# Optimization experiments

Hardware: AMD Instinct MI355X
Metric: run time of the kernel (lower is better)

Reference implementation:

```python
import jax, jax.numpy as jnp
import numpy as np

N = 50000      # nodes
E = 800000     # edges (avg degree 16)
F_IN = 512     # input features
H = 64         # hidden
C = 40         # classes
L = 4          # FAConv layers
EPS = 0.2      # args.epsilon


def setup_inputs() -> dict:
    key = jax.random.key(0)
    ks = jax.random.split(key, 8)
    gain = 1.414
    x = jax.random.normal(ks[0], (N, F_IN), jnp.float32)
    edge_index = jax.random.randint(ks[1], (2, E), 0, N, dtype=jnp.int32)
    W1 = jax.random.normal(ks[2], (H, F_IN), jnp.float32) * (gain * np.sqrt(2.0 / (F_IN + H)))
    b1 = jnp.zeros((H,), jnp.float32)
    W2 = jax.random.normal(ks[3], (C, H), jnp.float32) * (gain * np.sqrt(2.0 / (H + C)))
    b2 = jnp.zeros((C,), jnp.float32)
    att_l = jax.random.normal(ks[4], (L, H), jnp.float32) * np.sqrt(2.0 / (1 + H))
    att_r = jax.random.normal(ks[5], (L, H), jnp.float32) * np.sqrt(2.0 / (1 + H))
    return {"x": x, "edge_index": edge_index, "W1": W1, "b1": b1,
            "W2": W2, "b2": b2, "att_l": att_l, "att_r": att_r}


def reference(x, edge_index, W1, b1, W2, b2, att_l, att_r):
    n = x.shape[0]
    src, dst = edge_index[0], edge_index[1]
    # gcn_norm with self-loops (FAConv normalize=True, add_self_loops=True)
    loop = jnp.arange(n, dtype=src.dtype)
    rows = jnp.concatenate([src, loop])  # source j
    cols = jnp.concatenate([dst, loop])  # target i
    deg = jax.ops.segment_sum(jnp.ones_like(cols, dtype=x.dtype), cols, num_segments=n)
    dinv = jnp.where(deg > 0, jax.lax.rsqrt(jnp.maximum(deg, 1e-12)), 0.0)
    norm = dinv[rows] * dinv[cols]  # [E+N]

    # lin1 + relu (dropout inactive in eval)
    h = jax.nn.relu(x @ W1.T + b1)
    raw = h
    for l in range(L):
        al = h @ att_l[l]  # [N] per-source score
        ar = h @ att_r[l]  # [N] per-target score
        a = jnp.tanh(al[rows] + ar[cols])          # [E+N]
        msg = h[rows] * (a * norm)[:, None]        # [E+N, H]
        h = jax.ops.segment_sum(msg, cols, num_segments=n) + EPS * raw
    logits = h @ W2.T + b2
    return jax.nn.log_softmax(logits, axis=1)
```

## Files before the change

kernel.cpp:

```cpp
#include <hip/hip_runtime.h>

#define F_IN 512
#define HDIM 64
#define NCLS 40
#define NLAYER 4
#define EPS_F 0.2f

typedef __attribute__((ext_vector_type(8))) short short8;
typedef __attribute__((ext_vector_type(4))) float f32x4;
typedef __attribute__((ext_vector_type(8))) unsigned short ushort8;
typedef unsigned long long u64;

__device__ __forceinline__ unsigned short f2bf(float f) {
  unsigned u = __float_as_uint(f);
  u += 0x7FFFu + ((u >> 16) & 1u);
  return (unsigned short)(u >> 16);
}
__device__ __forceinline__ float bf2f(unsigned short s) {
  return __uint_as_float(((unsigned)s) << 16);
}
__device__ __forceinline__ float ftanh(float x) {
  float e = __expf(2.0f * x);
  return fmaf(-2.0f, __builtin_amdgcn_rcpf(e + 1.0f), 1.0f);
}

__global__ __launch_bounds__(256) void k_init(int* indeg, int nN) {
  int i = blockIdx.x * 256 + threadIdx.x;
  if (i < nN) indeg[i] = 0;
}

__global__ __launch_bounds__(256) void k_hist(const int* __restrict__ dst, int* indeg,
                                              int* __restrict__ rank, int nE) {
  int e = blockIdx.x * 256 + threadIdx.x;
  if (e < nE) rank[e] = atomicAdd(&indeg[dst[e]], 1);
}

__global__ __launch_bounds__(256) void k_bsum(const int* __restrict__ indeg, int* bsum, int nN) {
  int i0 = blockIdx.x * 512 + threadIdx.x;
  int v = 0;
  if (i0 < nN) v += indeg[i0];
  if (i0 + 256 < nN) v += indeg[i0 + 256];
#pragma unroll
  for (int off = 32; off > 0; off >>= 1) v += __shfl_xor(v, off, 64);
  __shared__ int s[4];
  if ((threadIdx.x & 63) == 0) s[threadIdx.x >> 6] = v;
  __syncthreads();
  if (threadIdx.x == 0) bsum[blockIdx.x] = s[0] + s[1] + s[2] + s[3];
}

__global__ __launch_bounds__(128) void k_bscan(const int* __restrict__ bsum, int* bpre,
                                               int* rowptr, int nblk, int nN, int nE) {
  __shared__ int sb[128];
  int t = threadIdx.x;
  int v = (t < nblk) ? bsum[t] : 0;
  sb[t] = v;
  __syncthreads();
  int acc = v;
  for (int off = 1; off < 128; off <<= 1) {
    int o = (t >= off) ? sb[t - off] : 0;
    __syncthreads();
    acc += o;
    sb[t] = acc;
    __syncthreads();
  }
  if (t < nblk) bpre[t] = acc - v;
  if (t == 0) rowptr[nN] = nE;
}

__global__ __launch_bounds__(512) void k_rowptr(const int* __restrict__ indeg,
                                                const int* __restrict__ bpre,
                                                const float* __restrict__ al,
                                                const float* __restrict__ ar,
                                                int* rowptr,
                                                float2* P, float2* Q, float* selfc, int nN) {
  __shared__ int sb[512];
  int t = threadIdx.x;
  int i = blockIdx.x * 512 + t;
  int v = (i < nN) ? indeg[i] : 0;
  sb[t] = v;
  __syncthreads();
  int acc = v;
  for (int off = 1; off < 512; off <<= 1) {
    int o = (t >= off) ? sb[t - off] : 0;
    __syncthreads();
    acc += o;
    sb[t] = acc;
    __syncthreads();
  }
  if (i < nN) {
    rowptr[i] = bpre[blockIdx.x] + acc - v;
    float dv = rsqrtf((float)v + 1.0f);
    float a = al[i], r = ar[i];
    P[i] = make_float2(a, dv);
    Q[i] = make_float2(r, dv);
    selfc[i] = tanhf(a + r) * dv * dv;
  }
}

__global__ __launch_bounds__(256) void k_scatter(const int* __restrict__ src,
                                                 const int* __restrict__ dst,
                                                 const int* __restrict__ rank,
                                                 const int* __restrict__ rowptr,
                                                 int* __restrict__ csrsrc, int nE) {
  int e = blockIdx.x * 256 + threadIdx.x;
  if (e < nE) {
    int d = dst[e];
    csrsrc[rowptr[d] + rank[e]] = src[e];
  }
}

__global__ __launch_bounds__(256) void k_lin1(const float* __restrict__ x,
                                              const float* __restrict__ W1,
                                              const float* __restrict__ b1,
                                              const float* __restrict__ attl0,
                                              const float* __restrict__ attr0,
                                              unsigned short* __restrict__ hraw,
                                              float* __restrict__ al, float* __restrict__ ar,
                                              int nN) {
  __shared__ unsigned short xs[64 * 64];
  __shared__ unsigned short ws[64 * 64];
  const int t = threadIdx.x;
  const int wv = t >> 6;
  const int l = t & 63;
  const int n0 = blockIdx.x * 64;
  const int srow = t >> 2;
  const int sk4 = (t & 3) * 4;
  const bool xvalid = (n0 + srow) < nN;
  const f32x4* x4 = reinterpret_cast<const f32x4*>(x);
  const f32x4* w4 = reinterpret_cast<const f32x4*>(W1);
  short8* xs8 = reinterpret_cast<short8*>(xs);
  short8* ws8 = reinterpret_cast<short8*>(ws);
  const int wslot0 = srow * 8 + (((t & 3) * 2 + 0) ^ (srow & 7));
  const int wslot1 = srow * 8 + (((t & 3) * 2 + 1) ^ (srow & 7));
  const int arow = l & 15;
  const int kgrp = l >> 4;
  f32x4 acc[4] = {{0.f, 0.f, 0.f, 0.f},
                  {0.f, 0.f, 0.f, 0.f},
                  {0.f, 0.f, 0.f, 0.f},
                  {0.f, 0.f, 0.f, 0.f}};
  f32x4 xa[4], wa[4];
  const f32x4 zero4 = {0.f, 0.f, 0.f, 0.f};
  {
    const size_t xb = (size_t)(n0 + srow) * (F_IN / 4) + sk4;
    const size_t wb = (size_t)srow * (F_IN / 4) + sk4;
#pragma unroll
    for (int r = 0; r < 4; ++r) {
      xa[r] = xvalid ? x4[xb + r] : zero4;
      wa[r] = w4[wb + r];
    }
  }
  for (int c = 0; c < 8; ++c) {
    short8 p0, p1, q0, q1;
#pragma unroll
    for (int r = 0; r < 2; ++r) {
#pragma unroll
      for (int j = 0; j < 4; ++j) {
        p0[r * 4 + j] = (short)f2bf(xa[r][j]);
        p1[r * 4 + j] = (short)f2bf(xa[2 + r][j]);
        q0[r * 4 + j] = (short)f2bf(wa[r][j]);
        q1[r * 4 + j] = (short)f2bf(wa[2 + r][j]);
      }
    }
    xs8[wslot0] = p0;
    xs8[wslot1] = p1;
    ws8[wslot0] = q0;
    ws8[wslot1] = q1;
    __syncthreads();
    if (c < 7) {
      const size_t xb = (size_t)(n0 + srow) * (F_IN / 4) + (c + 1) * 16 + sk4;
      const size_t wb = (size_t)srow * (F_IN / 4) + (c + 1) * 16 + sk4;
#pragma unroll
      for (int r = 0; r < 4; ++r) {
        xa[r] = xvalid ? x4[xb + r] : zero4;
        wa[r] = w4[wb + r];
      }
    }
#pragma unroll
    for (int c2 = 0; c2 < 2; ++c2) {
      const short8 a = xs8[(wv * 16 + arow) * 8 + ((c2 * 4 + kgrp) ^ (arow & 7))];
#pragma unroll
      for (int fs = 0; fs < 4; ++fs) {
        const short8 b = ws8[(fs * 16 + arow) * 8 + ((c2 * 4 + kgrp) ^ (arow & 7))];
        acc[fs] = __builtin_amdgcn_mfma_f32_16x16x32_bf16(a, b, acc[fs], 0, 0, 0);
      }
    }
    __syncthreads();
  }
  float psl[4] = {0.f, 0.f, 0.f, 0.f};
  float psr[4] = {0.f, 0.f, 0.f, 0.f};
#pragma unroll
  for (int fs = 0; fs < 4; ++fs) {
    const int feat = fs * 16 + arow;
    const float bias = b1[feat];
    const float atl = attl0[feat];
    const float atr = attr0[feat];
#pragma unroll
    for (int j = 0; j < 4; ++j) {
      const float v = fmaxf(acc[fs][j] + bias, 0.f);
      const int node = n0 + wv * 16 + kgrp * 4 + j;
      if (node < nN) hraw[(size_t)node * HDIM + feat] = f2bf(v);
      psl[j] = fmaf(v, atl, psl[j]);
      psr[j] = fmaf(v, atr, psr[j]);
    }
  }
#pragma unroll
  for (int off = 1; off <= 8; off <<= 1) {
#pragma unroll
    for (int j = 0; j < 4; ++j) {
      psl[j] += __shfl_xor(psl[j], off, 64);
      psr[j] += __shfl_xor(psr[j], off, 64);
    }
  }
  if (arow == 0) {
#pragma unroll
    for (int j = 0; j < 4; ++j) {
      const int node = n0 + wv * 16 + kgrp * 4 + j;
      if (node < nN) {
        al[node] = psl[j];
        ar[node] = psr[j];
      }
    }
  }
}

template <bool WNEXT>
__global__ __launch_bounds__(256) void k_agg(const unsigned short* __restrict__ h,
                                             const unsigned short* __restrict__ hraw,
                                             const int* __restrict__ rowptr,
                                             const int* __restrict__ csrsrc,
                                             const float2* __restrict__ Pc,
                                             const float2* __restrict__ Qc,
                                             const float* __restrict__ Sc,
                                             const float* __restrict__ attl_n,
                                             const float* __restrict__ attr_n,
                                             float2* __restrict__ Pn, float2* __restrict__ Qn,
                                             float* __restrict__ Sn,
                                             unsigned short* __restrict__ hout, int nN) {
  const int wid = threadIdx.x >> 6, lane = threadIdx.x & 63;
  const int dA = blockIdx.x * 8 + wid * 2;
  if (dA >= nN) return;
  const int dB = dA + 1;
  const bool hasB = dB < nN;
  const int dBs = hasB ? dB : dA;
  const int grp = lane >> 3;
  const int fo = (lane & 7) * 8;
  const size_t baseA = (size_t)dA * HDIM + fo;
  const size_t baseB = (size_t)dBs * HDIM + fo;
  const float2 qdA = Qc[dA];
  const float2 qdB = Qc[dBs];
  float accA[8] = {}, accB[8] = {};
  if (grp == 0) {
    const float sc = Sc[dA];
    const ushort8 hd = *reinterpret_cast<const ushort8*>(&h[baseA]);
    const ushort8 rw = *reinterpret_cast<const ushort8*>(&hraw[baseA]);
#pragma unroll
    for (int j = 0; j < 8; ++j) accA[j] = fmaf(bf2f(hd[j]), sc, EPS_F * bf2f(rw[j]));
  } else if (grp == 1 && hasB) {
    const float sc = Sc[dBs];
    const ushort8 hd = *reinterpret_cast<const ushort8*>(&h[baseB]);
    const ushort8 rw = *reinterpret_cast<const ushort8*>(&hraw[baseB]);
#pragma unroll
    for (int j = 0; j < 8; ++j) accB[j] = fmaf(bf2f(hd[j]), sc, EPS_F * bf2f(rw[j]));
  }
  const int r1A = rowptr[dA + 1];
  const int r1B = rowptr[dBs + 1];
  int eA = rowptr[dA] + grp;
  int eB = hasB ? (rowptr[dBs] + grp) : r1B;
  int sA = csrsrc[(eA < r1A) ? eA : 0];
  int sB = csrsrc[(eB < r1B) ? eB : 0];
  while (eA < r1A || eB < r1B) {
    const bool vA = eA < r1A;
    const bool vB = eB < r1B;
    const float2 pA = Pc[sA];
    const float2 pB = Pc[sB];
    const ushort8 hA = *reinterpret_cast<const ushort8*>(&h[(size_t)sA * HDIM + fo]);
    const ushort8 hB = *reinterpret_cast<const ushort8*>(&h[(size_t)sB * HDIM + fo]);
    const int eA2 = eA + 8;
    const int eB2 = eB + 8;
    const int sA2 = csrsrc[(eA2 < r1A) ? eA2 : 0];
    const int sB2 = csrsrc[(eB2 < r1B) ? eB2 : 0];
    const float cA = vA ? ftanh(pA.x + qdA.x) * (pA.y * qdA.y) : 0.f;
    const float cB = vB ? ftanh(pB.x + qdB.x) * (pB.y * qdB.y) : 0.f;
#pragma unroll
    for (int j = 0; j < 8; ++j) accA[j] = fmaf(bf2f(hA[j]), cA, accA[j]);
#pragma unroll
    for (int j = 0; j < 8; ++j) accB[j] = fmaf(bf2f(hB[j]), cB, accB[j]);
    eA = eA2;
    eB = eB2;
    sA = sA2;
    sB = sB2;
  }
#pragma unroll
  for (int off = 8; off <= 32; off <<= 1) {
#pragma unroll
    for (int j = 0; j < 8; ++j) {
      accA[j] += __shfl_xor(accA[j], off, 64);
      accB[j] += __shfl_xor(accB[j], off, 64);
    }
  }
  if (grp == 0) {
    ushort8 o;
#pragma unroll
    for (int j = 0; j < 8; ++j) o[j] = f2bf(accA[j]);
    *reinterpret_cast<ushort8*>(&hout[baseA]) = o;
  } else if (grp == 1 && hasB) {
    ushort8 o;
#pragma unroll
    for (int j = 0; j < 8; ++j) o[j] = f2bf(accB[j]);
    *reinterpret_cast<ushort8*>(&hout[baseB]) = o;
  }
  if (WNEXT) {
    float pslA = 0.f, psrA = 0.f, pslB = 0.f, psrB = 0.f;
#pragma unroll
    for (int j = 0; j < 8; ++j) {
      const float wl = attl_n[fo + j];
      const float wr = attr_n[fo + j];
      pslA = fmaf(accA[j], wl, pslA);
      psrA = fmaf(accA[j], wr, psrA);
      pslB = fmaf(accB[j], wl, pslB);
      psrB = fmaf(accB[j], wr, psrB);
    }
#pragma unroll
    for (int off = 1; off <= 4; off <<= 1) {
      pslA += __shfl_xor(pslA, off, 64);
      psrA += __shfl_xor(psrA, off, 64);
      pslB += __shfl_xor(pslB, off, 64);
      psrB += __shfl_xor(psrB, off, 64);
    }
    if (lane == 0) {
      Pn[dA] = make_float2(pslA, qdA.y);
      Qn[dA] = make_float2(psrA, qdA.y);
      Sn[dA] = ftanh(pslA + psrA) * qdA.y * qdA.y;
      if (hasB) {
        Pn[dB] = make_float2(pslB, qdB.y);
        Qn[dB] = make_float2(psrB, qdB.y);
        Sn[dB] = ftanh(pslB + psrB) * qdB.y * qdB.y;
      }
    }
  }
}

__global__ __launch_bounds__(256) void k_out(const unsigned short* __restrict__ h,
                                             const float* __restrict__ W2,
                                             const float* __restrict__ b2,
                                             float* __restrict__ out, int nN) {
  __shared__ float w2s[NCLS * HDIM];
  __shared__ float b2s[NCLS];
  for (int i = threadIdx.x; i < NCLS * HDIM; i += 256) w2s[i] = W2[i];
  if (threadIdx.x < NCLS) b2s[threadIdx.x] = b2[threadIdx.x];
  __syncthreads();
  const int n = blockIdx.x * 256 + threadIdx.x;
  if (n >= nN) return;
  float hr[HDIM];
  const ushort8* hrow = reinterpret_cast<const ushort8*>(&h[(size_t)n * HDIM]);
#pragma unroll
  for (int r = 0; r < 8; ++r) {
    const ushort8 v = hrow[r];
#pragma unroll
    for (int j = 0; j < 8; ++j) hr[r * 8 + j] = bf2f(v[j]);
  }
  const float4* w2s4 = reinterpret_cast<const float4*>(w2s);
  float logits[NCLS];
  float m = -INFINITY;
#pragma unroll
  for (int c = 0; c < NCLS; ++c) {
    float a0 = 0.f, a1 = 0.f, a2 = 0.f, a3 = 0.f;
#pragma unroll
    for (int j4 = 0; j4 < HDIM / 4; j4 += 4) {
      const float4 w0 = w2s4[c * (HDIM / 4) + j4 + 0];
      const float4 w1 = w2s4[c * (HDIM / 4) + j4 + 1];
      const float4 w2v = w2s4[c * (HDIM / 4) + j4 + 2];
      const float4 w3 = w2s4[c * (HDIM / 4) + j4 + 3];
      const int j = j4 * 4;
      a0 = fmaf(hr[j + 0], w0.x, a0);  a0 = fmaf(hr[j + 1], w0.y, a0);
      a0 = fmaf(hr[j + 2], w0.z, a0);  a0 = fmaf(hr[j + 3], w0.w, a0);
      a1 = fmaf(hr[j + 4], w1.x, a1);  a1 = fmaf(hr[j + 5], w1.y, a1);
      a1 = fmaf(hr[j + 6], w1.z, a1);  a1 = fmaf(hr[j + 7], w1.w, a1);
      a2 = fmaf(hr[j + 8], w2v.x, a2); a2 = fmaf(hr[j + 9], w2v.y, a2);
      a2 = fmaf(hr[j + 10], w2v.z, a2); a2 = fmaf(hr[j + 11], w2v.w, a2);
      a3 = fmaf(hr[j + 12], w3.x, a3); a3 = fmaf(hr[j + 13], w3.y, a3);
      a3 = fmaf(hr[j + 14], w3.z, a3); a3 = fmaf(hr[j + 15], w3.w, a3);
    }
    const float lg = (a0 + a1) + (a2 + a3) + b2s[c];
    logits[c] = lg;
    m = fmaxf(m, lg);
  }
  float s = 0.f;
#pragma unroll
  for (int c = 0; c < NCLS; ++c) s += expf(logits[c] - m);
  const float lse = m + logf(s);
  float4* o4 = reinterpret_cast<float4*>(&out[(size_t)n * NCLS]);
#pragma unroll
  for (int c4 = 0; c4 < NCLS / 4; ++c4) {
    float4 o;
    o.x = logits[c4 * 4 + 0] - lse;
    o.y = logits[c4 * 4 + 1] - lse;
    o.z = logits[c4 * 4 + 2] - lse;
    o.w = logits[c4 * 4 + 3] - lse;
    o4[c4] = o;
  }
}

extern "C" void kernel_launch(void* const* d_in, const int* in_sizes, int n_in,
                              void* d_out, int out_size, void* d_ws, size_t ws_size,
                              hipStream_t stream) {
  const float* x = (const float*)d_in[0];
  const int* ei = (const int*)d_in[1];
  const float* W1 = (const float*)d_in[2];
  const float* b1 = (const float*)d_in[3];
  const float* W2 = (const float*)d_in[4];
  const float* b2 = (const float*)d_in[5];
  const float* attl = (const float*)d_in[6];
  const float* attr = (const float*)d_in[7];
  float* out = (float*)d_out;

  const int nN = in_sizes[0] / F_IN;
  const int nE = in_sizes[1] / 2;
  const int* src = ei;
  const int* dst = ei + nE;

  char* w = (char*)d_ws;
  size_t off = 0;
  auto alloc = [&](size_t bytes) {
    void* p = (void*)(w + off);
    off = (off + bytes + 255) & ~(size_t)255;
    return p;
  };
  unsigned short* hraw = (unsigned short*)alloc((size_t)nN * HDIM * 2);
  unsigned short* hA = (unsigned short*)alloc((size_t)nN * HDIM * 2);
  unsigned short* hB = (unsigned short*)alloc((size_t)nN * HDIM * 2);
  float2* P0 = (float2*)alloc((size_t)nN * 8);
  float2* Q0 = (float2*)alloc((size_t)nN * 8);
  float* S0 = (float*)alloc((size_t)nN * 4);
  float2* P1 = (float2*)alloc((size_t)nN * 8);
  float2* Q1 = (float2*)alloc((size_t)nN * 8);
  float* S1 = (float*)alloc((size_t)nN * 4);
  float* al = (float*)alloc((size_t)nN * 4);
  float* ar = (float*)alloc((size_t)nN * 4);
  int* indeg = (int*)alloc((size_t)nN * 4);
  int* rank = (int*)alloc((size_t)nE * 4);
  int* rowptr = (int*)alloc((size_t)(nN + 1) * 4);
  int* csrsrc = (int*)alloc((size_t)nE * 4);
  int* bsum = (int*)alloc(1024);
  int* bpre = (int*)alloc(1024);

  const int nb_n = (nN + 255) / 256;
  const int nb_e = (nE + 255) / 256;
  const int nblk = (nN + 511) / 512;
  const int nb8 = (nN + 7) / 8;

  k_lin1<<<(nN + 63) / 64, 256, 0, stream>>>(x, W1, b1, attl, attr, hraw, al, ar, nN);
  k_init<<<nb_n, 256, 0, stream>>>(indeg, nN);
  k_hist<<<nb_e, 256, 0, stream>>>(dst, indeg, rank, nE);
  k_bsum<<<nblk, 256, 0, stream>>>(indeg, bsum, nN);
  k_bscan<<<1, 128, 0, stream>>>(bsum, bpre, rowptr, nblk, nN, nE);
  k_rowptr<<<nblk, 512, 0, stream>>>(indeg, bpre, al, ar, rowptr, P0, Q0, S0, nN);
  k_scatter<<<nb_e, 256, 0, stream>>>(src, dst, rank, rowptr, csrsrc, nE);

  const unsigned short* hin = hraw;
  unsigned short* hout = hA;
  float2 *Pc = P0, *Qc = Q0, *Pn = P1, *Qn = Q1;
  float *Sc = S0, *Sn = S1;
  for (int l = 0; l < NLAYER; ++l) {
    if (l < NLAYER - 1) {
      k_agg<true><<<nb8, 256, 0, stream>>>(hin, hraw, rowptr, csrsrc, Pc, Qc, Sc,
                                           attl + (l + 1) * HDIM, attr + (l + 1) * HDIM,
                                           Pn, Qn, Sn, hout, nN);
    } else {
      k_agg<false><<<nb8, 256, 0, stream>>>(hin, hraw, rowptr, csrsrc, Pc, Qc, Sc,
                                            nullptr, nullptr, Pn, Qn, Sn, hout, nN);
    }
    hin = hout;
    hout = (hout == hA) ? hB : hA;
    float2* tp = Pc; Pc = Pn; Pn = tp;
    float2* tq = Qc; Qc = Qn; Qn = tq;
    float* ts = Sc; Sc = Sn; Sn = ts;
  }
  k_out<<<nb_n, 256, 0, stream>>>(hin, W2, b2, out, nN);
}
```

Measured before the change: 217.5 us.

## Split lin1 K-reduction across two half-blocks and scatter CSR in two destination passes

k_lin1 now runs 512 threads per block. Each half computes the MFMA partial product over half of the 512 input features, and the halves are combined through shared memory before bias, ReLU and the attention dot products. This doubles the waves available to hide latency on the memory-bound x read, at the cost of an extra reduction step and more shared memory. The CSR scatter is also split into two launches, each handling one half of the destination range, to narrow the write footprint of each pass, which adds a second full read of dst.

```diff
diff --git a/kernel.cpp b/kernel.cpp
--- a/kernel.cpp
+++ b/kernel.cpp
@@ -101,15 +101,16 @@
                                                  const int* __restrict__ dst,
                                                  const int* __restrict__ rank,
                                                  const int* __restrict__ rowptr,
-                                                 int* __restrict__ csrsrc, int nE) {
+                                                 int* __restrict__ csrsrc, int nE,
+                                                 int dlo, int dhi) {
   int e = blockIdx.x * 256 + threadIdx.x;
   if (e < nE) {
     int d = dst[e];
-    csrsrc[rowptr[d] + rank[e]] = src[e];
-  }
-}
-
-__global__ __launch_bounds__(256) void k_lin1(const float* __restrict__ x,
+    if (d >= dlo && d < dhi) csrsrc[rowptr[d] + rank[e]] = src[e];
+  }
+}
+
+__global__ __launch_bounds__(512) void k_lin1(const float* __restrict__ x,
                                               const float* __restrict__ W1,
                                               const float* __restrict__ b1,
                                               const float* __restrict__ attl0,
@@ -117,21 +118,24 @@
                                               unsigned short* __restrict__ hraw,
                                               float* __restrict__ al, float* __restrict__ ar,
                                               int nN) {
-  __shared__ unsigned short xs[64 * 64];
-  __shared__ unsigned short ws[64 * 64];
+  __shared__ unsigned short xs[2][64 * 64];
+  __shared__ unsigned short ws[2][64 * 64];
   const int t = threadIdx.x;
-  const int wv = t >> 6;
+  const int half = t >> 8;
+  const int th = t & 255;
+  const int wv = (t >> 6) & 3;
   const int l = t & 63;
   const int n0 = blockIdx.x * 64;
-  const int srow = t >> 2;
-  const int sk4 = (t & 3) * 4;
+  const int srow = th >> 2;
+  const int sk4 = (th & 3) * 4;
   const bool xvalid = (n0 + srow) < nN;
+  const int kb4 = half * 64;
   const f32x4* x4 = reinterpret_cast<const f32x4*>(x);
   const f32x4* w4 = reinterpret_cast<const f32x4*>(W1);
-  short8* xs8 = reinterpret_cast<short8*>(xs);
-  short8* ws8 = reinterpret_cast<short8*>(ws);
-  const int wslot0 = srow * 8 + (((t & 3) * 2 + 0) ^ (srow & 7));
-  const int wslot1 = srow * 8 + (((t & 3) * 2 + 1) ^ (srow & 7));
+  short8* xs8 = reinterpret_cast<short8*>(xs[half]);
+  short8* ws8 = reinterpret_cast<short8*>(ws[half]);
+  const int wslot0 = srow * 8 + (((th & 3) * 2 + 0) ^ (srow & 7));
+  const int wslot1 = srow * 8 + (((th & 3) * 2 + 1) ^ (srow & 7));
   const int arow = l & 15;
   const int kgrp = l >> 4;
   f32x4 acc[4] = {{0.f, 0.f, 0.f, 0.f},
@@ -141,15 +145,15 @@
   f32x4 xa[4], wa[4];
   const f32x4 zero4 = {0.f, 0.f, 0.f, 0.f};
   {
-    const size_t xb = (size_t)(n0 + srow) * (F_IN / 4) + sk4;
-    const size_t wb = (size_t)srow * (F_IN / 4) + sk4;
+    const size_t xb = (size_t)(n0 + srow) * (F_IN / 4) + kb4 + sk4;
+    const size_t wb = (size_t)srow * (F_IN / 4) + kb4 + sk4;
 #pragma unroll
     for (int r = 0; r < 4; ++r) {
       xa[r] = xvalid ? x4[xb + r] : zero4;
       wa[r] = w4[wb + r];
     }
   }
-  for (int c = 0; c < 8; ++c) {
+  for (int c = 0; c < 4; ++c) {
     short8 p0, p1, q0, q1;
 #pragma unroll
     for (int r = 0; r < 2; ++r) {
@@ -166,9 +170,9 @@
     ws8[wslot0] = q0;
     ws8[wslot1] = q1;
     __syncthreads();
-    if (c < 7) {
-      const size_t xb = (size_t)(n0 + srow) * (F_IN / 4) + (c + 1) * 16 + sk4;
-      const size_t wb = (size_t)srow * (F_IN / 4) + (c + 1) * 16 + sk4;
+    if (c < 3) {
+      const size_t xb = (size_t)(n0 + srow) * (F_IN / 4) + kb4 + (c + 1) * 16 + sk4;
+      const size_t wb = (size_t)srow * (F_IN / 4) + kb4 + (c + 1) * 16 + sk4;
 #pragma unroll
       for (int r = 0; r < 4; ++r) {
         xa[r] = xvalid ? x4[xb + r] : zero4;
@@ -186,38 +190,54 @@
     }
     __syncthreads();
   }
-  float psl[4] = {0.f, 0.f, 0.f, 0.f};
-  float psr[4] = {0.f, 0.f, 0.f, 0.f};
-#pragma unroll
-  for (int fs = 0; fs < 4; ++fs) {
-    const int feat = fs * 16 + arow;
-    const float bias = b1[feat];
-    const float atl = attl0[feat];
-    const float atr = attr0[feat];
-#pragma unroll
-    for (int j = 0; j < 4; ++j) {
-      const float v = fmaxf(acc[fs][j] + bias, 0.f);
-      const int node = n0 + wv * 16 + kgrp * 4 + j;
-      if (node < nN) hraw[(size_t)node * HDIM + feat] = f2bf(v);
-      psl[j] = fmaf(v, atl, psl[j]);
-      psr[j] = fmaf(v, atr, psr[j]);
-    }
-  }
-#pragma unroll
-  for (int off = 1; off <= 8; off <<= 1) {
-#pragma unroll
-    for (int j = 0; j < 4; ++j) {
-      psl[j] += __shfl_xor(psl[j], off, 64);
-      psr[j] += __shfl_xor(psr[j], off, 64);
-    }
-  }
-  if (arow == 0) {
-#pragma unroll
-    for (int j = 0; j < 4; ++j) {
-      const int node = n0 + wv * 16 + kgrp * 4 + j;
-      if (node < nN) {
-        al[node] = psl[j];
-        ar[node] = psr[j];
+  float* red = reinterpret_cast<float*>(xs);
+  if (half == 1) {
+#pragma unroll
+    for (int fs = 0; fs < 4; ++fs) {
+      const int feat = fs * 16 + arow;
+#pragma unroll
+      for (int j = 0; j < 4; ++j) {
+        const int r = wv * 16 + kgrp * 4 + j;
+        red[r * 64 + feat] = acc[fs][j];
+      }
+    }
+  }
+  __syncthreads();
+  if (half == 0) {
+    float psl[4] = {0.f, 0.f, 0.f, 0.f};
+    float psr[4] = {0.f, 0.f, 0.f, 0.f};
+#pragma unroll
+    for (int fs = 0; fs < 4; ++fs) {
+      const int feat = fs * 16 + arow;
+      const float bias = b1[feat];
+      const float atl = attl0[feat];
+      const float atr = attr0[feat];
+#pragma unroll
+      for (int j = 0; j < 4; ++j) {
+        const int r = wv * 16 + kgrp * 4 + j;
+        const float v = fmaxf(acc[fs][j] + red[r * 64 + feat] + bias, 0.f);
+        const int node = n0 + r;
+        if (node < nN) hraw[(size_t)node * HDIM + feat] = f2bf(v);
+        psl[j] = fmaf(v, atl, psl[j]);
+        psr[j] = fmaf(v, atr, psr[j]);
+      }
+    }
+#pragma unroll
+    for (int off = 1; off <= 8; off <<= 1) {
+#pragma unroll
+      for (int j = 0; j < 4; ++j) {
+        psl[j] += __shfl_xor(psl[j], off, 64);
+        psr[j] += __shfl_xor(psr[j], off, 64);
+      }
+    }
+    if (arow == 0) {
+#pragma unroll
+      for (int j = 0; j < 4; ++j) {
+        const int node = n0 + wv * 16 + kgrp * 4 + j;
+        if (node < nN) {
+          al[node] = psl[j];
+          ar[node] = psr[j];
+        }
       }
     }
   }
@@ -448,14 +468,16 @@
   const int nb_e = (nE + 255) / 256;
   const int nblk = (nN + 511) / 512;
   const int nb8 = (nN + 7) / 8;
-
-  k_lin1<<<(nN + 63) / 64, 256, 0, stream>>>(x, W1, b1, attl, attr, hraw, al, ar, nN);
+  const int nHalf = nN / 2;
+
+  k_lin1<<<(nN + 63) / 64, 512, 0, stream>>>(x, W1, b1, attl, attr, hraw, al, ar, nN);
   k_init<<<nb_n, 256, 0, stream>>>(indeg, nN);
   k_hist<<<nb_e, 256, 0, stream>>>(dst, indeg, rank, nE);
   k_bsum<<<nblk, 256, 0, stream>>>(indeg, bsum, nN);
   k_bscan<<<1, 128, 0, stream>>>(bsum, bpre, rowptr, nblk, nN, nE);
   k_rowptr<<<nblk, 512, 0, stream>>>(indeg, bpre, al, ar, rowptr, P0, Q0, S0, nN);
-  k_scatter<<<nb_e, 256, 0, stream>>>(src, dst, rank, rowptr, csrsrc, nE);
+  k_scatter<<<nb_e, 256, 0, stream>>>(src, dst, rank, rowptr, csrsrc, nE, 0, nHalf);
+  k_scatter<<<nb_e, 256, 0, stream>>>(src, dst, rank, rowptr, csrsrc, nE, nHalf, nN);
 
   const unsigned short* hin = hraw;
   unsigned short* hout = hA;
```

Result: no change. 221.8 us (+2.0%).
